# Kernel tuning notes

Hardware: AMD Instinct MI355X
Metric: run time of the kernel (lower is better)

The kernel has to match this reference:

```python
import jax, jax.numpy as jnp
import numpy as np

N, IN_DIM, OUT_DIM, H = 8192, 128, 128, 2
HD = OUT_DIM // H
NEG_SLOPE = 0.2


def setup_inputs() -> dict:
    key = jax.random.key(0)
    k1, k2, k3, k4, k5 = jax.random.split(key, 5)
    x = jax.random.normal(k1, (N, IN_DIM), dtype=jnp.float32)
    adj = jax.random.randint(k2, (N, N), 0, 2).astype(jnp.float32)
    W = jax.random.normal(k3, (IN_DIM, OUT_DIM), dtype=jnp.float32) / np.sqrt(IN_DIM)
    a_src = jax.random.normal(k4, (H, HD), dtype=jnp.float32) * 0.01
    a_dst = jax.random.normal(k5, (H, HD), dtype=jnp.float32) * 0.01
    return {"x": x, "adj": adj, "W": W, "a_src": a_src, "a_dst": a_dst}


def reference(x, adj, W, a_src, a_dst):
    # h: (N, H, HD)
    h = (x @ W).reshape(N, H, HD)
    # per-node additive score halves: (N, H)
    e_src = jnp.einsum('nhd,hd->nh', h, a_src)
    e_dst = jnp.einsum('nhd,hd->nh', h, a_dst)
    # attn logits: (N_i, N_j, H); torch code adds e_src[i] + e_dst[j]
    logits = jax.nn.leaky_relu(e_src[:, None, :] + e_dst[None, :, :], NEG_SLOPE)
    logits = jnp.where(adj[:, :, None] > 0, logits, -jnp.inf)
    # softmax over neighbor axis j (dim=1), matching F.softmax(attn, dim=1)
    attn = jax.nn.softmax(logits, axis=1)
    # dropout omitted (eval mode)
    out = jnp.einsum('ijh,jhd->ihd', attn, h).reshape(N, OUT_DIM)
    return out
```

## Files before the change

kernel.cpp:

```cpp
#include <hip/hip_runtime.h>
#include <hip/hip_bf16.h>

#define N 8192
#define IND 128
#define OUTD 128

typedef float f32x4 __attribute__((ext_vector_type(4)));
typedef short s16x8 __attribute__((ext_vector_type(8)));
typedef _Float16 f16;
typedef _Float16 f16x4 __attribute__((ext_vector_type(4)));

static __device__ inline unsigned short f2bf(float f) {
    union { float f; unsigned u; } v; v.f = f;
    unsigned u = v.u + 0x7fffu + ((v.u >> 16) & 1u);
    return (unsigned short)(u >> 16);
}
static __device__ inline float bf2f(unsigned short b) {
    union { unsigned u; float f; } v; v.u = ((unsigned)b) << 16;
    return v.f;
}

__global__ __launch_bounds__(256) void k1_xw(const float* __restrict__ x,
                                             const float* __restrict__ W,
                                             unsigned short* __restrict__ hT) {
    __shared__ unsigned short Wl[128 * 130];
    const int tid = threadIdx.x;
    {
        int k = tid >> 1, n0 = (tid & 1) * 64;
        const float4* src = (const float4*)(W + k * 128 + n0);
#pragma unroll
        for (int v = 0; v < 16; ++v) {
            float4 f = src[v];
            int base = k * 130 + n0 + v * 4;
            Wl[base + 0] = f2bf(f.x);
            Wl[base + 1] = f2bf(f.y);
            Wl[base + 2] = f2bf(f.z);
            Wl[base + 3] = f2bf(f.w);
        }
    }
    __syncthreads();
    const int wave = tid >> 6, lane = tid & 63;
    const int m = lane & 15, quad = lane >> 4;
    const int ibase = blockIdx.x * 64 + wave * 16;
    const int irow = ibase + m;

    f32x4 acc[8];
#pragma unroll
    for (int t = 0; t < 8; ++t) acc[t] = (f32x4){0.f, 0.f, 0.f, 0.f};

#pragma unroll
    for (int ks = 0; ks < 4; ++ks) {
        const int k0 = ks * 32 + quad * 8;
        const float4* xp = (const float4*)(x + (size_t)irow * 128 + k0);
        float4 xa = xp[0], xb = xp[1];
        s16x8 afrag;
        afrag[0] = (short)f2bf(xa.x); afrag[1] = (short)f2bf(xa.y);
        afrag[2] = (short)f2bf(xa.z); afrag[3] = (short)f2bf(xa.w);
        afrag[4] = (short)f2bf(xb.x); afrag[5] = (short)f2bf(xb.y);
        afrag[6] = (short)f2bf(xb.z); afrag[7] = (short)f2bf(xb.w);
#pragma unroll
        for (int nt = 0; nt < 8; ++nt) {
            const int n = nt * 16 + m;
            s16x8 bfrag;
#pragma unroll
            for (int j = 0; j < 8; ++j)
                bfrag[j] = (short)Wl[(k0 + j) * 130 + n];
            acc[nt] = __builtin_amdgcn_mfma_f32_16x16x32_bf16(afrag, bfrag, acc[nt], 0, 0, 0);
        }
    }
#pragma unroll
    for (int nt = 0; nt < 8; ++nt) {
        const int c = nt * 16 + m;
        const int i0 = ibase + quad * 4;
        ushort4 pk;
        pk.x = f2bf(acc[nt][0]); pk.y = f2bf(acc[nt][1]);
        pk.z = f2bf(acc[nt][2]); pk.w = f2bf(acc[nt][3]);
        *(ushort4*)(hT + (size_t)c * N + i0) = pk;
    }
}

__global__ __launch_bounds__(256) void k2_e(const unsigned short* __restrict__ hT,
                                            const float* __restrict__ a_src,
                                            const float* __restrict__ a_dst,
                                            float* __restrict__ As, float* __restrict__ Cs,
                                            float4* __restrict__ BD) {
    const int i = blockIdx.x * 256 + threadIdx.x;
    float es0 = 0.f, ed0 = 0.f, es1 = 0.f, ed1 = 0.f;
#pragma unroll 8
    for (int c = 0; c < 128; ++c) {
        float v = bf2f(hT[(size_t)c * N + i]);
        float as = a_src[c], ad = a_dst[c];
        if (c < 64) { es0 += v * as; ed0 += v * ad; }
        else        { es1 += v * as; ed1 += v * ad; }
    }
    As[i]     = __expf(es0);
    As[N + i] = __expf(es1);
    Cs[i]     = __expf(0.2f * es0);
    Cs[N + i] = __expf(0.2f * es1);
    float4 bd;
    bd.x = __expf(ed0); bd.y = __expf(0.2f * ed0);
    bd.z = __expf(ed1); bd.w = __expf(0.2f * ed1);
    BD[i] = bd;
}

__global__ __launch_bounds__(256, 4) void k3_main(const float* __restrict__ adj,
                                                  const unsigned short* __restrict__ hT,
                                                  const float* __restrict__ As,
                                                  const float* __restrict__ Cs,
                                                  const float4* __restrict__ BD,
                                                  f16* __restrict__ Up,
                                                  float* __restrict__ Lp,
                                                  int jlen) {
    const int tid = threadIdx.x;
    const int wave = tid >> 6, lane = tid & 63;
    const int m = lane & 15, quad = lane >> 4;
    const int ibase = blockIdx.x * 64 + wave * 16;
    const int irow = ibase + m;
    const int jc = blockIdx.y;
    const int j0 = jc * jlen;

    const float A0 = As[irow], C0 = Cs[irow];
    const float A1 = As[N + irow], C1 = Cs[N + irow];

    f32x4 acc[2][4];
#pragma unroll
    for (int h = 0; h < 2; ++h)
#pragma unroll
        for (int nt = 0; nt < 4; ++nt) acc[h][nt] = (f32x4){0.f, 0.f, 0.f, 0.f};
    float ls0 = 0.f, ls1 = 0.f;

    const float* adjrow = adj + (size_t)irow * N;
    const int steps = jlen >> 5;

#pragma unroll 2
    for (int s = 0; s < steps; ++s) {
        const int jq = j0 + s * 32 + quad * 8;
        float aj[8];
        *(float4*)(aj)     = *(const float4*)(adjrow + jq);
        *(float4*)(aj + 4) = *(const float4*)(adjrow + jq + 4);
        float4 bd[8];
#pragma unroll
        for (int jj = 0; jj < 8; ++jj) bd[jj] = BD[jq + jj];

        s16x8 p0, p1;
#pragma unroll
        for (int jj = 0; jj < 8; ++jj) {
            float w0 = fmaxf(A0 * bd[jj].x, C0 * bd[jj].y);
            float pv0 = aj[jj] * w0;
            ls0 += pv0;
            p0[jj] = (short)f2bf(pv0);
            float w1 = fmaxf(A1 * bd[jj].z, C1 * bd[jj].w);
            float pv1 = aj[jj] * w1;
            ls1 += pv1;
            p1[jj] = (short)f2bf(pv1);
        }
#pragma unroll
        for (int nt = 0; nt < 4; ++nt) {
            const int c0 = nt * 16 + m;
            s16x8 h0 = *(const s16x8*)(hT + (size_t)c0 * N + jq);
            s16x8 h1 = *(const s16x8*)(hT + (size_t)(c0 + 64) * N + jq);
            acc[0][nt] = __builtin_amdgcn_mfma_f32_16x16x32_bf16(p0, h0, acc[0][nt], 0, 0, 0);
            acc[1][nt] = __builtin_amdgcn_mfma_f32_16x16x32_bf16(p1, h1, acc[1][nt], 0, 0, 0);
        }
    }

    ls0 += __shfl_xor(ls0, 16, 64);
    ls0 += __shfl_xor(ls0, 32, 64);
    ls1 += __shfl_xor(ls1, 16, 64);
    ls1 += __shfl_xor(ls1, 32, 64);

    f16* Ub = Up + (size_t)jc * N * 128;
#pragma unroll
    for (int h = 0; h < 2; ++h)
#pragma unroll
        for (int nt = 0; nt < 4; ++nt) {
            const int c = h * 64 + nt * 16 + m;
            const int ib = ibase + quad * 4;
#pragma unroll
            for (int r = 0; r < 4; ++r)
                Ub[(size_t)(ib + r) * 128 + c] = (f16)acc[h][nt][r];
        }
    if (quad == 0) {
        Lp[((size_t)jc * 2 + 0) * N + irow] = ls0;
        Lp[((size_t)jc * 2 + 1) * N + irow] = ls1;
    }
}

__global__ __launch_bounds__(256) void k4_reduce(const f16* __restrict__ Up,
                                                 const float* __restrict__ Lp,
                                                 float* __restrict__ out, int JC) {
    const int base = (blockIdx.x * 256 + threadIdx.x) * 4;
    const int i = base >> 7, c = base & 127, h = c >> 6;
    float su0 = 0.f, su1 = 0.f, su2 = 0.f, su3 = 0.f, sl = 0.f;
    for (int jcc = 0; jcc < JC; ++jcc) {
        f16x4 u = *(const f16x4*)(Up + (size_t)jcc * N * 128 + base);
        su0 += (float)u[0]; su1 += (float)u[1];
        su2 += (float)u[2]; su3 += (float)u[3];
        sl += Lp[((size_t)jcc * 2 + h) * N + i];
    }
    float inv = 1.0f / sl;
    float4 o; o.x = su0 * inv; o.y = su1 * inv; o.z = su2 * inv; o.w = su3 * inv;
    *(float4*)(out + base) = o;
}

extern "C" void kernel_launch(void* const* d_in, const int* in_sizes, int n_in,
                              void* d_out, int out_size, void* d_ws, size_t ws_size,
                              hipStream_t stream) {
    const float* x     = (const float*)d_in[0];
    const float* adj   = (const float*)d_in[1];
    const float* W     = (const float*)d_in[2];
    const float* a_src = (const float*)d_in[3];
    const float* a_dst = (const float*)d_in[4];
    float* out = (float*)d_out;
    char* ws = (char*)d_ws;

    size_t off = 0;
    unsigned short* hT = (unsigned short*)(ws + off); off += (size_t)128 * N * 2;
    float* As = (float*)(ws + off); off += (size_t)2 * N * 4;
    float* Cs = (float*)(ws + off); off += (size_t)2 * N * 4;
    float4* BD = (float4*)(ws + off); off += (size_t)N * 16;

    int JC = 8;
    while (JC > 1) {
        size_t need = off + (size_t)JC * N * 128 * 2 + (size_t)JC * 2 * N * 4;
        if (need <= ws_size) break;
        JC >>= 1;
    }
    f16* Up = (f16*)(ws + off);
    float* Lp = (float*)(ws + off + (size_t)JC * N * 128 * 2);

    k1_xw<<<N / 64, 256, 0, stream>>>(x, W, hT);
    k2_e<<<N / 256, 256, 0, stream>>>(hT, a_src, a_dst, As, Cs, BD);
    dim3 g3(N / 64, JC);
    k3_main<<<g3, 256, 0, stream>>>(adj, hT, As, Cs, BD, Up, Lp, N / JC);
    k4_reduce<<<(N * 128) / (256 * 4), 256, 0, stream>>>(Up, Lp, out, JC);
}
```

Baseline: 542.4 us.

## Stage BD in LDS, prefetch next adj tile, hoist hT loads in main loop

```diff
diff --git a/kernel.cpp b/kernel.cpp
--- a/kernel.cpp
+++ b/kernel.cpp
@@ -4,6 +4,9 @@
 #define N 8192
 #define IND 128
 #define OUTD 128
+#define JC 8
+#define JLEN 1024
+#define STEPS 32
 
 typedef float f32x4 __attribute__((ext_vector_type(4)));
 typedef short s16x8 __attribute__((ext_vector_type(8)));
@@ -103,21 +106,23 @@
     BD[i] = bd;
 }
 
-__global__ __launch_bounds__(256, 4) void k3_main(const float* __restrict__ adj,
+__global__ __launch_bounds__(256, 3) void k3_main(const float* __restrict__ adj,
                                                   const unsigned short* __restrict__ hT,
                                                   const float* __restrict__ As,
                                                   const float* __restrict__ Cs,
                                                   const float4* __restrict__ BD,
                                                   f16* __restrict__ Up,
-                                                  float* __restrict__ Lp,
-                                                  int jlen) {
+                                                  float* __restrict__ Lp) {
+    __shared__ float4 BDl[JLEN + JLEN / 8];
     const int tid = threadIdx.x;
     const int wave = tid >> 6, lane = tid & 63;
     const int m = lane & 15, quad = lane >> 4;
     const int ibase = blockIdx.x * 64 + wave * 16;
     const int irow = ibase + m;
     const int jc = blockIdx.y;
-    const int j0 = jc * jlen;
+    const int j0 = jc * JLEN;
+
+    for (int t = tid; t < JLEN; t += 256) BDl[t + (t >> 3)] = BD[j0 + t];
 
     const float A0 = As[irow], C0 = Cs[irow];
     const float A1 = As[N + irow], C1 = Cs[N + irow];
@@ -130,38 +135,52 @@
     float ls0 = 0.f, ls1 = 0.f;
 
     const float* adjrow = adj + (size_t)irow * N;
-    const int steps = jlen >> 5;
-
-#pragma unroll 2
-    for (int s = 0; s < steps; ++s) {
+    __syncthreads();
+
+    float4 aja = *(const float4*)(adjrow + j0 + quad * 8);
+    float4 ajb = *(const float4*)(adjrow + j0 + quad * 8 + 4);
+
+#pragma unroll 1
+    for (int s = 0; s < STEPS; ++s) {
         const int jq = j0 + s * 32 + quad * 8;
-        float aj[8];
-        *(float4*)(aj)     = *(const float4*)(adjrow + jq);
-        *(float4*)(aj + 4) = *(const float4*)(adjrow + jq + 4);
-        float4 bd[8];
-#pragma unroll
-        for (int jj = 0; jj < 8; ++jj) bd[jj] = BD[jq + jj];
-
+
+        s16x8 h0[4], h1[4];
+#pragma unroll
+        for (int nt = 0; nt < 4; ++nt) {
+            h0[nt] = *(const s16x8*)(hT + (size_t)(nt * 16 + m) * N + jq);
+            h1[nt] = *(const s16x8*)(hT + (size_t)(nt * 16 + m + 64) * N + jq);
+        }
+
+        const int sn = (s + 1) & (STEPS - 1);
+        const int jqn = j0 + sn * 32 + quad * 8;
+        float4 ana = *(const float4*)(adjrow + jqn);
+        float4 anb = *(const float4*)(adjrow + jqn + 4);
+
+        const int bbase = s * 32 + quad * 8;
+        const int bidx = bbase + (bbase >> 3);
+        float ajv[8];
+        *(float4*)(ajv)     = aja;
+        *(float4*)(ajv + 4) = ajb;
         s16x8 p0, p1;
 #pragma unroll
         for (int jj = 0; jj < 8; ++jj) {
-            float w0 = fmaxf(A0 * bd[jj].x, C0 * bd[jj].y);
-            float pv0 = aj[jj] * w0;
+            float4 bd = BDl[bidx + jj];
+            float w0 = fmaxf(A0 * bd.x, C0 * bd.y);
+            float pv0 = ajv[jj] * w0;
             ls0 += pv0;
             p0[jj] = (short)f2bf(pv0);
-            float w1 = fmaxf(A1 * bd[jj].z, C1 * bd[jj].w);
-            float pv1 = aj[jj] * w1;
+            float w1 = fmaxf(A1 * bd.z, C1 * bd.w);
+            float pv1 = ajv[jj] * w1;
             ls1 += pv1;
             p1[jj] = (short)f2bf(pv1);
         }
+
 #pragma unroll
         for (int nt = 0; nt < 4; ++nt) {
-            const int c0 = nt * 16 + m;
-            s16x8 h0 = *(const s16x8*)(hT + (size_t)c0 * N + jq);
-            s16x8 h1 = *(const s16x8*)(hT + (size_t)(c0 + 64) * N + jq);
-            acc[0][nt] = __builtin_amdgcn_mfma_f32_16x16x32_bf16(p0, h0, acc[0][nt], 0, 0, 0);
-            acc[1][nt] = __builtin_amdgcn_mfma_f32_16x16x32_bf16(p1, h1, acc[1][nt], 0, 0, 0);
-        }
+            acc[0][nt] = __builtin_amdgcn_mfma_f32_16x16x32_bf16(p0, h0[nt], acc[0][nt], 0, 0, 0);
+            acc[1][nt] = __builtin_amdgcn_mfma_f32_16x16x32_bf16(p1, h1[nt], acc[1][nt], 0, 0, 0);
+        }
+        aja = ana; ajb = anb;
     }
 
     ls0 += __shfl_xor(ls0, 16, 64);
@@ -188,10 +207,11 @@
 
 __global__ __launch_bounds__(256) void k4_reduce(const f16* __restrict__ Up,
                                                  const float* __restrict__ Lp,
-                                                 float* __restrict__ out, int JC) {
+                                                 float* __restrict__ out) {
     const int base = (blockIdx.x * 256 + threadIdx.x) * 4;
     const int i = base >> 7, c = base & 127, h = c >> 6;
     float su0 = 0.f, su1 = 0.f, su2 = 0.f, su3 = 0.f, sl = 0.f;
+#pragma unroll
     for (int jcc = 0; jcc < JC; ++jcc) {
         f16x4 u = *(const f16x4*)(Up + (size_t)jcc * N * 128 + base);
         su0 += (float)u[0]; su1 += (float)u[1];
@@ -220,18 +240,12 @@
     float* Cs = (float*)(ws + off); off += (size_t)2 * N * 4;
     float4* BD = (float4*)(ws + off); off += (size_t)N * 16;
 
-    int JC = 8;
-    while (JC > 1) {
-        size_t need = off + (size_t)JC * N * 128 * 2 + (size_t)JC * 2 * N * 4;
-        if (need <= ws_size) break;
-        JC >>= 1;
-    }
     f16* Up = (f16*)(ws + off);
     float* Lp = (float*)(ws + off + (size_t)JC * N * 128 * 2);
 
     k1_xw<<<N / 64, 256, 0, stream>>>(x, W, hT);
     k2_e<<<N / 256, 256, 0, stream>>>(hT, a_src, a_dst, As, Cs, BD);
     dim3 g3(N / 64, JC);
-    k3_main<<<g3, 256, 0, stream>>>(adj, hT, As, Cs, BD, Up, Lp, N / JC);
-    k4_reduce<<<(N * 128) / (256 * 4), 256, 0, stream>>>(Up, Lp, out, JC);
-}
+    k3_main<<<g3, 256, 0, stream>>>(adj, hT, As, Cs, BD, Up, Lp);
+    k4_reduce<<<(N * 128) / (256 * 4), 256, 0, stream>>>(Up, Lp, out);
+}
```

Measured after the change: 538.9 us. No clear change (-0.6%).
